# Performance work log

Measured on AMD Instinct MI355X. Metric: run time of the kernel, lower is better.

## Reference

```python
import jax, jax.numpy as jnp
from jax import lax
import numpy as np

# cfg constants (not present in snippet; fixed realistic values)
GAMMA = 5.0            # cfg.RISK_AVERSION
COST_COEFF = 1e-3      # cfg.COST_COEFF
ALPHA = 0.95           # cfg.CVAR_CONFIDENCE
KAPPA = 2.0627128075074256  # norm.pdf(norm.ppf(0.95)) / (1 - 0.95)
PEN_XI = 100.0
N_ITERS = 500
LR = 0.01

B, H, N = 128, 12, 100


def setup_inputs() -> dict:
    key = jax.random.key(0)
    k1, k2, k3, k4 = jax.random.split(key, 4)
    mu = 0.02 * jax.random.normal(k1, (B, H, N), dtype=jnp.float32)
    # factor scale so that sigma_p = ||L^T w|| is O(0.02) for diversified w
    L = 0.02 * jax.random.normal(k2, (B, H, N, N), dtype=jnp.float32)
    w_prev = jax.random.uniform(k3, (B, N), dtype=jnp.float32)
    w_prev = w_prev / jnp.sum(w_prev, axis=-1, keepdims=True)  # on simplex
    cvar_limit = 0.05 + 0.05 * jax.random.uniform(k4, (B,), dtype=jnp.float32)
    return {"mu": mu, "L": L, "w_prev": w_prev, "cvar_limit": cvar_limit}


def _project_simplex(v):
    # Euclidean projection of each last-axis vector onto {w >= 0, sum w = 1}
    n = v.shape[-1]
    u = jnp.sort(v, axis=-1)[..., ::-1]
    cssv = jnp.cumsum(u, axis=-1) - 1.0
    ar = jnp.arange(1, n + 1, dtype=v.dtype)
    rho = jnp.sum(u * ar > cssv, axis=-1)          # >= 1 always
    theta = jnp.take_along_axis(cssv, (rho - 1)[..., None], axis=-1)
    theta = theta / rho[..., None].astype(v.dtype)
    return jnp.maximum(v - theta, 0.0)


def _neg_objective(w, mu, L, w_prev, cvar_limit):
    # w: (B,H,N). Exact-penalty reformulation: optimal xi_t = relu(-mu_p + kappa*sigma_p - limit)
    Lw = jnp.einsum('bhnm,bhn->bhm', L, w)             # L[t].T @ w[t]
    ret_t = jnp.einsum('bhn,bhn->bh', mu, w)           # mu[t] @ w[t]
    risk = jnp.sum(Lw * Lw, axis=(1, 2))               # sum_t ||L_t^T w_t||^2
    w_lag = jnp.concatenate([w_prev[:, None, :], w[:, :-1]], axis=1)
    diff = w - w_lag
    cost = jnp.sum(jnp.sqrt(diff * diff + 1e-10), axis=(1, 2))  # smoothed L1 turnover
    sigma = jnp.sqrt(jnp.sum(Lw * Lw, axis=-1) + 1e-12)          # (B,H)
    viol = jnp.maximum(-ret_t + KAPPA * sigma - cvar_limit[:, None], 0.0)
    obj = jnp.sum(ret_t, 1) - GAMMA * risk - COST_COEFF * cost - PEN_XI * jnp.sum(viol, 1)
    return -jnp.sum(obj)


def _solve(mu, L, w_prev, cvar_limit):
    b, h, n = mu.shape
    w0 = jnp.broadcast_to(w_prev[:, None, :], (b, h, n))
    grad_fn = jax.grad(_neg_objective)

    def step(w, _):
        g = grad_fn(w, mu, L, w_prev, cvar_limit)
        return _project_simplex(w - LR * g), None

    w, _ = lax.scan(jax.checkpoint(step), w0, None, length=N_ITERS)
    return w


def reference(mu, L, w_prev, cvar_limit):
    # Batched projected-gradient solver for the same convex MPO program the
    # original solves with SCS via CvxpyLayer; returns the optimal plan w (B,H,N).
    return _solve(mu, L, w_prev, cvar_limit)
```

## Files before the change

### kernel.cpp

```cpp
#include <hip/hip_runtime.h>
#include <cstdint>
#include <cstddef>

#define NIT    500
#define GAMMA_ 5.0f
#define CC_    1e-3f
#define KAPPA_ 2.0627128075074256f
#define PEN_   100.0f
#define LR_    0.01f

#define PBUF_BYTES (128*2*2*100*4)
#define FLAG_COUNT 256

#define VMFENCE() asm volatile("s_waitcnt vmcnt(0)" ::: "memory")
__device__ __forceinline__ float sysLoadF(float* p) {
  return __hip_atomic_load(p, __ATOMIC_RELAXED, __HIP_MEMORY_SCOPE_SYSTEM);
}
__device__ __forceinline__ void sysStoreF(float* p, float v) {
  __hip_atomic_store(p, v, __ATOMIC_RELAXED, __HIP_MEMORY_SCOPE_SYSTEM);
}
__device__ __forceinline__ int sysLoadI(int* p) {
  return __hip_atomic_load(p, __ATOMIC_RELAXED, __HIP_MEMORY_SCOPE_SYSTEM);
}
__device__ __forceinline__ void sysStoreI(int* p, int v) {
  __hip_atomic_store(p, v, __ATOMIC_RELAXED, __HIP_MEMORY_SCOPE_SYSTEM);
}
__device__ __forceinline__ int flagRead(int* p, int lane) {
  int f = 0;
  if (lane == 0) f = sysLoadI(p);
  return __builtin_amdgcn_readfirstlane(f);
}
__device__ __forceinline__ int ldsLoadAcq(int* p) {
  return __hip_atomic_load(p, __ATOMIC_ACQUIRE, __HIP_MEMORY_SCOPE_WORKGROUP);
}
__device__ __forceinline__ void ldsStoreRel(int* p, int v) {
  __hip_atomic_store(p, v, __ATOMIC_RELEASE, __HIP_MEMORY_SCOPE_WORKGROUP);
}

__device__ __forceinline__ float rdlane(float v, int lane) {
  return __int_as_float(__builtin_amdgcn_readlane(__float_as_int(v), lane));
}

__device__ __forceinline__ float wred64(float x) {
  int t;
  t = __builtin_amdgcn_update_dpp(0, __float_as_int(x), 0x111, 0xf, 0xf, true); x += __int_as_float(t);
  t = __builtin_amdgcn_update_dpp(0, __float_as_int(x), 0x112, 0xf, 0xf, true); x += __int_as_float(t);
  t = __builtin_amdgcn_update_dpp(0, __float_as_int(x), 0x114, 0xf, 0xf, true); x += __int_as_float(t);
  t = __builtin_amdgcn_update_dpp(0, __float_as_int(x), 0x118, 0xf, 0xf, true); x += __int_as_float(t);
  t = __builtin_amdgcn_update_dpp(0, __float_as_int(x), 0x142, 0xa, 0xf, true); x += __int_as_float(t);
  t = __builtin_amdgcn_update_dpp(0, __float_as_int(x), 0x143, 0xc, 0xf, true); x += __int_as_float(t);
  return rdlane(x, 63);
}

__global__ __launch_bounds__(768, 1) void mpo_solver(
    const float* __restrict__ mu, const float* __restrict__ L,
    const float* __restrict__ wprev, const float* __restrict__ climit,
    float* __restrict__ out, float* __restrict__ pbuf, int* __restrict__ flags)
{
  const int tid  = threadIdx.x;
  const int lane = tid & 63;
  const int wave = __builtin_amdgcn_readfirstlane(tid >> 6);
  const int j    = wave >> 1;
  const int sec  = wave & 1;
  const int bid  = blockIdx.x;
  const int b    = bid & 127;
  const int half = bid >> 7;
  const int h    = half * 6 + j;
  const int bh   = b * 12 + h;

  __shared__ float wbuf[2][6][100];
  __shared__ float ybuf[6][100];
  __shared__ float nbuf[100];
  __shared__ int   nflag;

  const float* Lb = L + (size_t)bh * 10000;

  float S[100];
#pragma unroll
  for (int c = 0; c < 100; ++c) S[c] = 0.f;
  const int r = sec * 50 + lane;
  if (lane < 50) {
#pragma unroll 1
    for (int mc = 0; mc < 25; ++mc) {
      float4 lr = *(const float4*)(Lb + r * 100 + mc * 4);
#pragma unroll
      for (int c = 0; c < 100; ++c) {
        const float* Lc = Lb + c * 100 + mc * 4;
        S[c] = fmaf(lr.x, Lc[0], fmaf(lr.y, Lc[1], fmaf(lr.z, Lc[2], fmaf(lr.w, Lc[3], S[c]))));
      }
    }
  }

  const bool val1 = (lane < 36);
  float mu0 = mu[(size_t)bh * 100 + lane];
  float mu1 = val1 ? mu[(size_t)bh * 100 + 64 + lane] : 0.f;
  float wp0 = wprev[b * 100 + lane];
  float wp1 = val1 ? wprev[b * 100 + 64 + lane] : 0.f;
  float lim = climit[b];

  float w0 = wp0, w1 = wp1;

  if (sec == 0) {
    wbuf[0][j][lane] = wp0;
    if (val1) wbuf[0][j][64 + lane] = wp1;
  }
  if (tid == 0) nflag = 0;
  __syncthreads();

  const bool hasNext = (h < 11);
  const bool isPubL  = (half == 0) && (j == 5);
  const bool isPubH  = (half == 1) && (j == 0);
  const bool isBnd   = isPubL || isPubH;
  const int  flagPub = isPubL ? (b * 2 + 0) : (b * 2 + 1);
  const int  flagCon = isPubL ? (b * 2 + 1) : (b * 2 + 0);
  bool dead = false;
  float thp = -3.0e38f;

  for (int k = 0; k < NIT; ++k) {
    const int p = k & 1;

    float yloc;
    {
      float a0 = 0.f, a1 = 0.f, a2 = 0.f, a3 = 0.f;
      const float* wrow = wbuf[p][j];
#pragma unroll
      for (int q = 0; q < 25; ++q) {
        float4 wq = *(const float4*)(wrow + q * 4);
        a0 = fmaf(wq.x, S[q * 4 + 0], a0);
        a1 = fmaf(wq.y, S[q * 4 + 1], a1);
        a2 = fmaf(wq.z, S[q * 4 + 2], a2);
        a3 = fmaf(wq.w, S[q * 4 + 3], a3);
      }
      yloc = (a0 + a2) + (a1 + a3);
      if (sec == 1 && lane < 50) ybuf[j][50 + lane] = yloc;
    }
    __syncthreads();

    if (sec == 1) {
      if (isBnd && k > 0) {
        if (!dead) {
          long guard = 0;
          while (flagRead(&flags[flagCon], lane) < k) {
            __builtin_amdgcn_s_sleep(1);
            if (++guard > (1L << 18)) { dead = true; break; }
          }
        }
        float* src = pbuf + ((size_t)flagCon * 2 + (k & 1)) * 100;
        nbuf[lane] = sysLoadF(&src[lane]);
        if (val1) nbuf[64 + lane] = sysLoadF(&src[64 + lane]);
        if (lane == 0) {  }
        ldsStoreRel(&nflag, k);
      }
    } else {
      float y0 = (lane < 50) ? yloc : ybuf[j][lane];
      float y1 = val1 ? ybuf[j][64 + lane] : 0.f;

      float ret = wred64(fmaf(mu0, w0, mu1 * w1));
      float s2  = wred64(fmaf(y0, w0, y1 * w1));
      float sigma = sqrtf(s2 + 1e-12f);
      float z     = KAPPA_ * sigma - ret - lim;
      float act   = (z > 0.f) ? 1.f : 0.f;
      float cY    = 2.f * GAMMA_ + act * (PEN_ * KAPPA_ / sigma);
      float cM    = -(1.f + act * PEN_);

      float wl0, wl1, wn0 = 0.f, wn1 = 0.f;
      if (j == 0) {
        if (half == 0 || k == 0) { wl0 = wp0; wl1 = wp1; }
        else {
          if (!dead) {
            long guard = 0;
            while (ldsLoadAcq(&nflag) < k) {
              __builtin_amdgcn_s_sleep(1);
              if (++guard > (1L << 18)) { dead = true; break; }
            }
          }
          wl0 = nbuf[lane];
          wl1 = val1 ? nbuf[64 + lane] : 0.f;
        }
      } else { wl0 = wbuf[p][j - 1][lane]; wl1 = val1 ? wbuf[p][j - 1][64 + lane] : 0.f; }
      if (hasNext) {
        if (j == 5) {
          if (k == 0) { wn0 = wp0; wn1 = wp1; }
          else {
            if (!dead) {
              long guard = 0;
              while (ldsLoadAcq(&nflag) < k) {
                __builtin_amdgcn_s_sleep(1);
                if (++guard > (1L << 18)) { dead = true; break; }
              }
            }
            wn0 = nbuf[lane];
            wn1 = val1 ? nbuf[64 + lane] : 0.f;
          }
        } else { wn0 = wbuf[p][j + 1][lane]; wn1 = val1 ? wbuf[p][j + 1][64 + lane] : 0.f; }
      }

      float dw0 = w0 - wl0;
      float g0  = fmaf(cM, mu0, cY * y0) + CC_ * (dw0 * rsqrtf(fmaf(dw0, dw0, 1e-10f)));
      if (hasNext) { float dn0 = wn0 - w0; g0 -= CC_ * (dn0 * rsqrtf(fmaf(dn0, dn0, 1e-10f))); }
      float v0 = fmaf(-LR_, g0, w0);
      float v1 = 0.f;
      if (val1) {
        float dw1 = w1 - wl1;
        float g1  = fmaf(cM, mu1, cY * y1) + CC_ * (dw1 * rsqrtf(fmaf(dw1, dw1, 1e-10f)));
        if (hasNext) { float dn1 = wn1 - w1; g1 -= CC_ * (dn1 * rsqrtf(fmaf(dn1, dn1, 1e-10f))); }
        v1 = fmaf(-LR_, g1, w1);
      }

      float a1m = val1 ? 1.f : 0.f;
      float na0 = (v0 > thp) ? 1.f : 0.f;
      float na1 = (val1 && (v1 > thp)) ? 1.f : 0.f;
      float Ssum = wred64(na0 * v0 + na1 * v1);
      float Cnt  = wred64(na0 + na1);
      if (Cnt < 0.5f) { Ssum = wred64(v0 + a1m * v1); Cnt = 100.f; }
      float theta = (Ssum - 1.f) / Cnt;
      for (int it = 0; it < 112; ++it) {
        na0 = (v0 > theta) ? 1.f : 0.f;
        na1 = (val1 && (v1 > theta)) ? 1.f : 0.f;
        float ns = wred64(na0 * v0 + na1 * v1);
        float nc = wred64(na0 + na1);
        if (nc == Cnt && ns == Ssum) break;
        if (it == 7) {
          ns = wred64(v0 + a1m * v1);
          nc = 100.f;
        }
        Ssum = ns; Cnt = nc;
        theta = (Ssum - 1.f) / Cnt;
      }
      thp = theta;
      w0 = fmaxf(v0 - theta, 0.f);
      w1 = val1 ? fmaxf(v1 - theta, 0.f) : 0.f;

      wbuf[1 - p][j][lane] = w0;
      if (val1) wbuf[1 - p][j][64 + lane] = w1;

      if (isBnd) {
        float* dst = pbuf + ((size_t)flagPub * 2 + ((k + 1) & 1)) * 100;
        sysStoreF(&dst[lane], w0);
        if (val1) sysStoreF(&dst[64 + lane], w1);
        VMFENCE();
        if (lane == 0) sysStoreI(&flags[flagPub], k + 1);
      }
    }
    __syncthreads();
  }

  if (sec == 0) {
    float* o = out + (size_t)bh * 100;
    o[lane] = w0;
    if (val1) o[64 + lane] = w1;
  }
}

extern "C" void kernel_launch(void* const* d_in, const int* in_sizes, int n_in,
                              void* d_out, int out_size, void* d_ws, size_t ws_size,
                              hipStream_t stream) {
  const float* mu = (const float*)d_in[0];
  const float* L  = (const float*)d_in[1];
  const float* wp = (const float*)d_in[2];
  const float* cl = (const float*)d_in[3];
  float* pbuf  = (float*)d_ws;
  int*   flags = (int*)((char*)d_ws + PBUF_BYTES);
  hipMemsetAsync(flags, 0, FLAG_COUNT * sizeof(int), stream);
  hipLaunchKernelGGL(mpo_solver, dim3(256), dim3(768), 0, stream,
                     mu, L, wp, cl, (float*)d_out, pbuf, flags);
}
```

Baseline: 1.651 ms.

## Replace block-wide barriers with per-wave LDS flags and triple-buffered weights

Drops both per-iteration __syncthreads and replaces them with point-to-point LDS release/acquire flags: a ybuf-ready flag per horizon and a w-ready flag per horizon. The weight buffer becomes triple-buffered so neighbouring waves can run up to an iteration apart without overwriting data still being read. The intent is to stop the whole 12-wave block from waiting on the slowest wave, since the projection loop runs a variable number of iterations per wave. In exchange it adds spin-wait polling with sleeps, which costs extra instructions and carries memory-ordering risk.

```diff
diff --git a/kernel.cpp b/kernel.cpp
--- a/kernel.cpp
+++ b/kernel.cpp
@@ -51,6 +51,17 @@
   t = __builtin_amdgcn_update_dpp(0, __float_as_int(x), 0x143, 0xc, 0xf, true); x += __int_as_float(t);
   return rdlane(x, 63);
 }
+
+#define SPIN_LDS(PTR, TGT)                                                   \
+  do {                                                                       \
+    if (!dead) {                                                             \
+      long guard_ = 0;                                                       \
+      while (ldsLoadAcq(PTR) < (TGT)) {                                      \
+        __builtin_amdgcn_s_sleep(1);                                         \
+        if (++guard_ > (1L << 18)) { dead = true; break; }                   \
+      }                                                                      \
+    }                                                                        \
+  } while (0)
 
 __global__ __launch_bounds__(768, 1) void mpo_solver(
     const float* __restrict__ mu, const float* __restrict__ L,
@@ -68,10 +79,12 @@
   const int h    = half * 6 + j;
   const int bh   = b * 12 + h;
 
-  __shared__ float wbuf[2][6][100];
+  __shared__ float wbuf[3][6][100];
   __shared__ float ybuf[6][100];
   __shared__ float nbuf[100];
   __shared__ int   nflag;
+  __shared__ int   yflag[6];
+  __shared__ int   wflag[6];
 
   const float* Lb = L + (size_t)bh * 10000;
 
@@ -104,7 +117,8 @@
     wbuf[0][j][lane] = wp0;
     if (val1) wbuf[0][j][64 + lane] = wp1;
   }
-  if (tid == 0) nflag = 0;
+  if (tid < 6) { yflag[tid] = -1; wflag[tid] = 0; }
+  if (tid == 6) nflag = 0;
   __syncthreads();
 
   const bool hasNext = (h < 11);
@@ -117,7 +131,9 @@
   float thp = -3.0e38f;
 
   for (int k = 0; k < NIT; ++k) {
-    const int p = k & 1;
+    const int p = k - (k / 3) * 3;
+
+    if (sec == 1 && k > 0) SPIN_LDS(&wflag[j], k);
 
     float yloc;
     {
@@ -132,11 +148,12 @@
         a3 = fmaf(wq.w, S[q * 4 + 3], a3);
       }
       yloc = (a0 + a2) + (a1 + a3);
-      if (sec == 1 && lane < 50) ybuf[j][50 + lane] = yloc;
     }
-    __syncthreads();
 
     if (sec == 1) {
+      if (lane < 50) ybuf[j][50 + lane] = yloc;
+      ldsStoreRel(&yflag[j], k);
+
       if (isBnd && k > 0) {
         if (!dead) {
           long guard = 0;
@@ -148,14 +165,15 @@
         float* src = pbuf + ((size_t)flagCon * 2 + (k & 1)) * 100;
         nbuf[lane] = sysLoadF(&src[lane]);
         if (val1) nbuf[64 + lane] = sysLoadF(&src[64 + lane]);
-        if (lane == 0) {  }
         ldsStoreRel(&nflag, k);
       }
     } else {
+      float ret = wred64(fmaf(mu0, w0, mu1 * w1));
+
+      SPIN_LDS(&yflag[j], k);
       float y0 = (lane < 50) ? yloc : ybuf[j][lane];
       float y1 = val1 ? ybuf[j][64 + lane] : 0.f;
 
-      float ret = wred64(fmaf(mu0, w0, mu1 * w1));
       float s2  = wred64(fmaf(y0, w0, y1 * w1));
       float sigma = sqrtf(s2 + 1e-12f);
       float z     = KAPPA_ * sigma - ret - lim;
@@ -167,32 +185,28 @@
       if (j == 0) {
         if (half == 0 || k == 0) { wl0 = wp0; wl1 = wp1; }
         else {
-          if (!dead) {
-            long guard = 0;
-            while (ldsLoadAcq(&nflag) < k) {
-              __builtin_amdgcn_s_sleep(1);
-              if (++guard > (1L << 18)) { dead = true; break; }
-            }
-          }
+          SPIN_LDS(&nflag, k);
           wl0 = nbuf[lane];
           wl1 = val1 ? nbuf[64 + lane] : 0.f;
         }
-      } else { wl0 = wbuf[p][j - 1][lane]; wl1 = val1 ? wbuf[p][j - 1][64 + lane] : 0.f; }
+      } else {
+        SPIN_LDS(&wflag[j - 1], k);
+        wl0 = wbuf[p][j - 1][lane];
+        wl1 = val1 ? wbuf[p][j - 1][64 + lane] : 0.f;
+      }
       if (hasNext) {
         if (j == 5) {
           if (k == 0) { wn0 = wp0; wn1 = wp1; }
           else {
-            if (!dead) {
-              long guard = 0;
-              while (ldsLoadAcq(&nflag) < k) {
-                __builtin_amdgcn_s_sleep(1);
-                if (++guard > (1L << 18)) { dead = true; break; }
-              }
-            }
+            SPIN_LDS(&nflag, k);
             wn0 = nbuf[lane];
             wn1 = val1 ? nbuf[64 + lane] : 0.f;
           }
-        } else { wn0 = wbuf[p][j + 1][lane]; wn1 = val1 ? wbuf[p][j + 1][64 + lane] : 0.f; }
+        } else {
+          SPIN_LDS(&wflag[j + 1], k);
+          wn0 = wbuf[p][j + 1][lane];
+          wn1 = val1 ? wbuf[p][j + 1][64 + lane] : 0.f;
+        }
       }
 
       float dw0 = w0 - wl0;
@@ -231,8 +245,10 @@
       w0 = fmaxf(v0 - theta, 0.f);
       w1 = val1 ? fmaxf(v1 - theta, 0.f) : 0.f;
 
-      wbuf[1 - p][j][lane] = w0;
-      if (val1) wbuf[1 - p][j][64 + lane] = w1;
+      int pn = p + 1; if (pn == 3) pn = 0;
+      wbuf[pn][j][lane] = w0;
+      if (val1) wbuf[pn][j][64 + lane] = w1;
+      ldsStoreRel(&wflag[j], k + 1);
 
       if (isBnd) {
         float* dst = pbuf + ((size_t)flagPub * 2 + ((k + 1) & 1)) * 100;
@@ -242,7 +258,6 @@
         if (lane == 0) sysStoreI(&flags[flagPub], k + 1);
       }
     }
-    __syncthreads();
   }
 
   if (sec == 0) {
```

Result: slower. 1.714 ms (+3.8%).

## Split each batch's horizon across four blocks with single-buffered ack handshakes

Applied to the files above, without the earlier changes.

Each batch's 12-step horizon is now spread over 4 blocks of 3 steps (512 blocks of 384 threads) instead of 2 blocks of 6 steps. Interior blocks exchange boundary weights with both neighbours through global buffers, and a new ack flag replaces the old double buffering. The goal is to use more CUs and give each block less serial work per iteration. The cost is more cross-block synchronization per iteration, since every boundary wave must now wait on an ack before publishing.

```diff
diff --git a/kernel.cpp b/kernel.cpp
--- a/kernel.cpp
+++ b/kernel.cpp
@@ -9,8 +9,8 @@
 #define PEN_   100.0f
 #define LR_    0.01f
 
-#define PBUF_BYTES (128*2*2*100*4)
-#define FLAG_COUNT 256
+#define PBUF_BYTES (128*6*100*4)
+#define FLAG_COUNT 1536
 
 #define VMFENCE() asm volatile("s_waitcnt vmcnt(0)" ::: "memory")
 __device__ __forceinline__ float sysLoadF(float* p) {
@@ -52,7 +52,29 @@
   return rdlane(x, 63);
 }
 
-__global__ __launch_bounds__(768, 1) void mpo_solver(
+#define SPIN_LDS(PTR, TGT)                                                   \
+  do {                                                                       \
+    if (!dead) {                                                             \
+      long guard_ = 0;                                                       \
+      while (ldsLoadAcq(PTR) < (TGT)) {                                      \
+        __builtin_amdgcn_s_sleep(1);                                         \
+        if (++guard_ > (1L << 18)) { dead = true; break; }                   \
+      }                                                                      \
+    }                                                                        \
+  } while (0)
+
+#define SPIN_SYS(PTR, TGT)                                                   \
+  do {                                                                       \
+    if (!dead) {                                                             \
+      long guard_ = 0;                                                       \
+      while (flagRead((PTR), lane) < (TGT)) {                                \
+        __builtin_amdgcn_s_sleep(1);                                         \
+        if (++guard_ > (1L << 18)) { dead = true; break; }                   \
+      }                                                                      \
+    }                                                                        \
+  } while (0)
+
+__global__ __launch_bounds__(384, 1) void mpo_solver(
     const float* __restrict__ mu, const float* __restrict__ L,
     const float* __restrict__ wprev, const float* __restrict__ climit,
     float* __restrict__ out, float* __restrict__ pbuf, int* __restrict__ flags)
@@ -63,15 +85,17 @@
   const int j    = wave >> 1;
   const int sec  = wave & 1;
   const int bid  = blockIdx.x;
-  const int b    = bid & 127;
-  const int half = bid >> 7;
-  const int h    = half * 6 + j;
+  const int b    = bid >> 2;
+  const int q    = bid & 3;
+  const int h    = q * 3 + j;
   const int bh   = b * 12 + h;
-
-  __shared__ float wbuf[2][6][100];
-  __shared__ float ybuf[6][100];
-  __shared__ float nbuf[100];
-  __shared__ int   nflag;
+  int* acks = flags + 768;
+
+  __shared__ float wbuf[2][3][100];
+  __shared__ float ybuf[3][100];
+  __shared__ float nbufL[100];
+  __shared__ float nbufR[100];
+  __shared__ int   nflagL, nflagR;
 
   const float* Lb = L + (size_t)bh * 10000;
 
@@ -104,15 +128,15 @@
     wbuf[0][j][lane] = wp0;
     if (val1) wbuf[0][j][64 + lane] = wp1;
   }
-  if (tid == 0) nflag = 0;
+  if (tid == 0) { nflagL = 0; nflagR = 0; }
   __syncthreads();
 
   const bool hasNext = (h < 11);
-  const bool isPubL  = (half == 0) && (j == 5);
-  const bool isPubH  = (half == 1) && (j == 0);
-  const bool isBnd   = isPubL || isPubH;
-  const int  flagPub = isPubL ? (b * 2 + 0) : (b * 2 + 1);
-  const int  flagCon = isPubL ? (b * 2 + 1) : (b * 2 + 0);
+  const bool conL = (j == 0) && (q > 0);
+  const bool conR = (j == 2) && (q < 3);
+  const bool isBnd = conL || conR;
+  const int  dirConsume = conL ? (b * 6 + (q - 1) * 2 + 0) : (b * 6 + q * 2 + 1);
+  const int  dirPublish = conL ? (b * 6 + (q - 1) * 2 + 1) : (b * 6 + q * 2 + 0);
   bool dead = false;
   float thp = -3.0e38f;
 
@@ -124,12 +148,12 @@
       float a0 = 0.f, a1 = 0.f, a2 = 0.f, a3 = 0.f;
       const float* wrow = wbuf[p][j];
 #pragma unroll
-      for (int q = 0; q < 25; ++q) {
-        float4 wq = *(const float4*)(wrow + q * 4);
-        a0 = fmaf(wq.x, S[q * 4 + 0], a0);
-        a1 = fmaf(wq.y, S[q * 4 + 1], a1);
-        a2 = fmaf(wq.z, S[q * 4 + 2], a2);
-        a3 = fmaf(wq.w, S[q * 4 + 3], a3);
+      for (int qq = 0; qq < 25; ++qq) {
+        float4 wq = *(const float4*)(wrow + qq * 4);
+        a0 = fmaf(wq.x, S[qq * 4 + 0], a0);
+        a1 = fmaf(wq.y, S[qq * 4 + 1], a1);
+        a2 = fmaf(wq.z, S[qq * 4 + 2], a2);
+        a3 = fmaf(wq.w, S[qq * 4 + 3], a3);
       }
       yloc = (a0 + a2) + (a1 + a3);
       if (sec == 1 && lane < 50) ybuf[j][50 + lane] = yloc;
@@ -138,18 +162,21 @@
 
     if (sec == 1) {
       if (isBnd && k > 0) {
-        if (!dead) {
-          long guard = 0;
-          while (flagRead(&flags[flagCon], lane) < k) {
-            __builtin_amdgcn_s_sleep(1);
-            if (++guard > (1L << 18)) { dead = true; break; }
-          }
+        SPIN_SYS(&flags[dirConsume], k);
+        float* src = pbuf + (size_t)dirConsume * 100;
+        float x0 = sysLoadF(&src[lane]);
+        float x1 = val1 ? sysLoadF(&src[64 + lane]) : 0.f;
+        if (conL) {
+          nbufL[lane] = x0;
+          if (val1) nbufL[64 + lane] = x1;
+          ldsStoreRel(&nflagL, k);
+        } else {
+          nbufR[lane] = x0;
+          if (val1) nbufR[64 + lane] = x1;
+          ldsStoreRel(&nflagR, k);
         }
-        float* src = pbuf + ((size_t)flagCon * 2 + (k & 1)) * 100;
-        nbuf[lane] = sysLoadF(&src[lane]);
-        if (val1) nbuf[64 + lane] = sysLoadF(&src[64 + lane]);
-        if (lane == 0) {  }
-        ldsStoreRel(&nflag, k);
+        VMFENCE();
+        if (lane == 0) sysStoreI(&acks[dirConsume], k);
       }
     } else {
       float y0 = (lane < 50) ? yloc : ybuf[j][lane];
@@ -165,32 +192,20 @@
 
       float wl0, wl1, wn0 = 0.f, wn1 = 0.f;
       if (j == 0) {
-        if (half == 0 || k == 0) { wl0 = wp0; wl1 = wp1; }
+        if (q == 0 || k == 0) { wl0 = wp0; wl1 = wp1; }
         else {
-          if (!dead) {
-            long guard = 0;
-            while (ldsLoadAcq(&nflag) < k) {
-              __builtin_amdgcn_s_sleep(1);
-              if (++guard > (1L << 18)) { dead = true; break; }
-            }
-          }
-          wl0 = nbuf[lane];
-          wl1 = val1 ? nbuf[64 + lane] : 0.f;
+          SPIN_LDS(&nflagL, k);
+          wl0 = nbufL[lane];
+          wl1 = val1 ? nbufL[64 + lane] : 0.f;
         }
       } else { wl0 = wbuf[p][j - 1][lane]; wl1 = val1 ? wbuf[p][j - 1][64 + lane] : 0.f; }
       if (hasNext) {
-        if (j == 5) {
+        if (j == 2) {
           if (k == 0) { wn0 = wp0; wn1 = wp1; }
           else {
-            if (!dead) {
-              long guard = 0;
-              while (ldsLoadAcq(&nflag) < k) {
-                __builtin_amdgcn_s_sleep(1);
-                if (++guard > (1L << 18)) { dead = true; break; }
-              }
-            }
-            wn0 = nbuf[lane];
-            wn1 = val1 ? nbuf[64 + lane] : 0.f;
+            SPIN_LDS(&nflagR, k);
+            wn0 = nbufR[lane];
+            wn1 = val1 ? nbufR[64 + lane] : 0.f;
           }
         } else { wn0 = wbuf[p][j + 1][lane]; wn1 = val1 ? wbuf[p][j + 1][64 + lane] : 0.f; }
       }
@@ -234,12 +249,13 @@
       wbuf[1 - p][j][lane] = w0;
       if (val1) wbuf[1 - p][j][64 + lane] = w1;
 
-      if (isBnd) {
-        float* dst = pbuf + ((size_t)flagPub * 2 + ((k + 1) & 1)) * 100;
+      if (isBnd && k < NIT - 1) {
+        SPIN_SYS(&acks[dirPublish], k);
+        float* dst = pbuf + (size_t)dirPublish * 100;
         sysStoreF(&dst[lane], w0);
         if (val1) sysStoreF(&dst[64 + lane], w1);
         VMFENCE();
-        if (lane == 0) sysStoreI(&flags[flagPub], k + 1);
+        if (lane == 0) sysStoreI(&flags[dirPublish], k + 1);
       }
     }
     __syncthreads();
@@ -262,6 +278,6 @@
   float* pbuf  = (float*)d_ws;
   int*   flags = (int*)((char*)d_ws + PBUF_BYTES);
   hipMemsetAsync(flags, 0, FLAG_COUNT * sizeof(int), stream);
-  hipLaunchKernelGGL(mpo_solver, dim3(256), dim3(768), 0, stream,
+  hipLaunchKernelGGL(mpo_solver, dim3(512), dim3(384), 0, stream,
                      mu, L, wp, cl, (float*)d_out, pbuf, flags);
 }
```

After: 3.454 ms. 2.09x slower.
